# Kernel tuning notes

Hardware: AMD Instinct MI355X
Metric: run time of the kernel (lower is better)

The kernel has to match this reference:

```python
import jax, jax.numpy as jnp
import numpy as np

E = 2        # expan_att_chans
HEADS = 16   # num_chans * expan_att_chans


def _gconv1x1(x, w, b, groups):
    # Grouped 1x1 conv. x: [B, Cin, H, W]; w: [Cout, Cin//groups]; b: [Cout].
    # Output channel layout matches torch: group-major (c_group * gout + o).
    B, Cin, H, W = x.shape
    Cout = w.shape[0]
    gin, gout = Cin // groups, Cout // groups
    y = jnp.einsum('bgip,goi->bgop',
                   x.reshape(B, groups, gin, H * W),
                   w.reshape(groups, gout, gin))
    return y.reshape(B, Cout, H, W) + b[None, :, None, None]


def _l2norm(x, eps=1e-12):
    # F.normalize(dim=-1): x / max(||x||_2, eps)
    n = jnp.sqrt(jnp.sum(x * x, axis=-1, keepdims=True))
    return x / jnp.maximum(n, eps)


def setup_inputs() -> dict:
    key = jax.random.key(0)
    ks = jax.random.split(key, 12)
    B, C, H, W = 8, 128, 128, 128
    s = 0.05  # small init (module uses xavier gain=0.01)
    f32 = jnp.float32
    return {
        'x': jax.random.normal(ks[0], (B, C, H, W), f32),
        'to': jax.random.normal(ks[1], (B, C, H, W), f32),
        't': jnp.ones((1, HEADS, 1, 1), f32),
        # rgb qkv chain (fusion): C -> 2EC -> EC -> EC, all groups=C
        'w_r1': (jax.random.normal(ks[2], (C * E * 2, 1), f32) * s),
        'b_r1': jnp.zeros((C * E * 2,), f32),
        'w_r2': (jax.random.normal(ks[3], (C * E, 2 * E), f32) * s),
        'b_r2': jnp.zeros((C * E,), f32),
        'w_r3': (jax.random.normal(ks[4], (C * E, E), f32) * s),
        'b_r3': jnp.zeros((C * E,), f32),
        # text kv chain: C -> 2EC -> EC -> 2EC, all groups=C
        'w_t1': (jax.random.normal(ks[5], (C * E * 2, 1), f32) * s),
        'b_t1': jnp.zeros((C * E * 2,), f32),
        'w_t2': (jax.random.normal(ks[6], (C * E, 2 * E), f32) * s),
        'b_t2': jnp.zeros((C * E,), f32),
        'w_t3': (jax.random.normal(ks[7], (C * E * 2, E), f32) * s),
        'b_t3': jnp.zeros((C * E * 2,), f32),
        # fusion conv: Conv2d(E*C -> C, k=3, stride=1, pad=1) + LeakyReLU(0.2)
        'w_f': (jax.random.normal(ks[8], (C, C * E, 3, 3), f32) * 0.02),
        'b_f': jnp.zeros((C,), f32),
    }


def reference(x, to, t, w_r1, b_r1, w_r2, b_r2, w_r3, b_r3,
              w_t1, b_t1, w_t2, b_t2, w_t3, b_t3, w_f, b_f):
    B, C, H, W = x.shape
    Cexp = E * C
    d = Cexp // HEADS  # per-head channel dim
    HW = H * W

    # grouped 1x1 conv chains producing Q (from rgb) and K,V (from text)
    q = _gconv1x1(_gconv1x1(_gconv1x1(x, w_r1, b_r1, C), w_r2, b_r2, C), w_r3, b_r3, C)      # [B, EC, H, W]
    kv = _gconv1x1(_gconv1x1(_gconv1x1(to, w_t1, b_t1, C), w_t2, b_t2, C), w_t3, b_t3, C)    # [B, 2EC, H, W]

    # Rearrange 'B (C E) H W -> B E C H W' then view as [B, heads, d, HW]
    q = q.reshape(B, C, E, HW).transpose(0, 2, 1, 3).reshape(B, HEADS, d, HW)
    kv = kv.reshape(B, C, 2 * E, HW).transpose(0, 2, 1, 3)  # [B, 2E, C, HW]
    k = kv[:, :E].reshape(B, HEADS, d, HW)
    v = kv[:, E:].reshape(B, HEADS, d, HW)

    # channel (transposed) attention with L2-normalized Q,K and learned temperature
    qn, kn = _l2norm(q), _l2norm(k)
    attn = jax.nn.softmax(jnp.einsum('bhdp,bhep->bhde', qn, kn) * t, axis=-1)  # [B, H, d, d]
    xo = jnp.einsum('bhde,bhep->bhdp', attn, v)  # [B, heads, d, HW]

    # rearrange 'B C X (H W) -> B (X C) H W' with C=heads, X=d  (d-major, head-minor)
    xo = xo.transpose(0, 2, 1, 3).reshape(B, Cexp, H, W)

    # group_fus: 3x3 conv (stride 1, pad 1) + LeakyReLU(0.2), residual add
    y = jax.lax.conv_general_dilated(
        xo, w_f, window_strides=(1, 1), padding=((1, 1), (1, 1)),
        dimension_numbers=('NCHW', 'OIHW', 'NCHW'))
    y = jax.nn.leaky_relu(y + b_f[None, :, None, None], negative_slope=0.2)
    return x + y
```

## Files before the change

kernel.cpp:

```cpp
#include <hip/hip_runtime.h>
#include <math.h>

#define B_  8
#define C_  128
#define H_  128
#define W_  128
#define HW_ 16384

#define OFF_MPART 0
#define OFF_SPART 262144
#define OFF_M     327680
#define OFF_S     344064
#define OFF_WV    348160
#define OFF_CST   380928
#define OFF_T     382976
#define OFF_WEFF  392192
#define OFF_T2F   982016
#define T2_ROW    16640
#define T2_BATCH  2163200
#define WS_NEED   (982016ull * 4ull + 34611200ull)

typedef __attribute__((ext_vector_type(8))) short short8;
typedef __attribute__((ext_vector_type(4))) float f32x4;

__device__ __forceinline__ unsigned short f2bf(float f) {
  unsigned u = __float_as_uint(f);
  u += 0x7fffu + ((u >> 16) & 1u);
  return (unsigned short)(u >> 16);
}

__device__ __forceinline__ f32x4 mfma16(short8 a, short8 b, f32x4 c) {
  return __builtin_amdgcn_mfma_f32_16x16x32_bf16(a, b, c, 0, 0, 0);
}

__device__ __forceinline__ void gl16(const void* g, void* l) {
  const unsigned loff = (unsigned)(unsigned long long)l;
  __builtin_amdgcn_global_load_lds(
      (const __attribute__((address_space(1))) void*)g,
      (__attribute__((address_space(3))) void*)loff, 16, 0, 0);
}

__global__ __launch_bounds__(256) void k_gram(const float* __restrict__ x,
                                              const float* __restrict__ to,
                                              float* __restrict__ ws) {
  const int bid = blockIdx.x;
  const int ps  = bid & 15;
  const int blk = (bid >> 4) & 7;
  const int b   = bid >> 7;
  const int tid = threadIdx.x;
  const int w = tid >> 6, l = tid & 63;
  const int lm = l & 15, lh = l >> 4;
  const int c0 = blk * 16;

  const float* xc = x  + ((size_t)b * C_ + c0 + lm) * HW_;
  const float* tc = to + ((size_t)b * C_ + c0 + lm) * HW_;
  const int p0 = ps * 1024 + w * 256 + lh * 8;

  f32x4 acc = (f32x4)0.f;
  float sx = 0.f, sxx = 0.f, st = 0.f, stt = 0.f;
#pragma unroll
  for (int it = 0; it < 8; ++it) {
    const int p = p0 + it * 32;
    const f32x4 xa = *(const f32x4*)(xc + p);
    const f32x4 xb = *(const f32x4*)(xc + p + 4);
    const f32x4 ta = *(const f32x4*)(tc + p);
    const f32x4 tb = *(const f32x4*)(tc + p + 4);
    short8 xf, tf;
#pragma unroll
    for (int e = 0; e < 4; ++e) {
      xf[e]     = (short)f2bf(xa[e]);
      xf[4 + e] = (short)f2bf(xb[e]);
      tf[e]     = (short)f2bf(ta[e]);
      tf[4 + e] = (short)f2bf(tb[e]);
      sx += xa[e] + xb[e];
      sxx = fmaf(xa[e], xa[e], fmaf(xb[e], xb[e], sxx));
      st += ta[e] + tb[e];
      stt = fmaf(ta[e], ta[e], fmaf(tb[e], tb[e], stt));
    }
    acc = mfma16(xf, tf, acc);
  }

  sx  += __shfl_xor(sx, 16);  sx  += __shfl_xor(sx, 32);
  sxx += __shfl_xor(sxx, 16); sxx += __shfl_xor(sxx, 32);
  st  += __shfl_xor(st, 16);  st  += __shfl_xor(st, 32);
  stt += __shfl_xor(stt, 16); stt += __shfl_xor(stt, 32);

  __shared__ float smM[4][256];
  __shared__ float smS[4][4][16];
#pragma unroll
  for (int r = 0; r < 4; ++r)
    smM[w][(lh * 4 + r) * 16 + lm] = acc[r];
  if (l < 16) {
    smS[w][0][lm] = sx;  smS[w][1][lm] = sxx;
    smS[w][2][lm] = st;  smS[w][3][lm] = stt;
  }
  __syncthreads();

  {
    const float s = smM[0][tid & 255] + smM[1][tid & 255]
                  + smM[2][tid & 255] + smM[3][tid & 255];
    ws[OFF_MPART + (size_t)((b * 8 + blk) * 16 + ps) * 256 + tid] = s;
  }
  if (tid < 64) {
    const int kind = tid >> 4, ch = tid & 15;
    const float s = smS[0][kind][ch] + smS[1][kind][ch]
                  + smS[2][kind][ch] + smS[3][kind][ch];
    ws[OFF_SPART + (size_t)kind * 16384 + (size_t)(b * C_ + c0 + ch) * 16 + ps] = s;
  }
}

__global__ __launch_bounds__(256) void k_redB(float* __restrict__ ws) {
  const int gid = blockIdx.x * 256 + threadIdx.x;
  if (gid < 16384) {
    const float* mp = ws + OFF_MPART + (size_t)(gid >> 8) * 4096 + (gid & 255);
    float s = 0.f;
#pragma unroll
    for (int kc = 0; kc < 16; ++kc) s += mp[kc * 256];
    ws[OFF_M + gid] = s;
  } else {
    const int sidx = gid - 16384;
    const float* sp = ws + OFF_SPART + (size_t)sidx * 16;
    float s = 0.f;
#pragma unroll
    for (int kc = 0; kc < 16; ++kc) s += sp[kc];
    ws[OFF_S + sidx] = s;
  }
}

__global__ __launch_bounds__(256) void k_zero(unsigned short* __restrict__ t2) {
  const int b = blockIdx.x >> 1, r = blockIdx.x & 1;
  unsigned short* row = t2 + (size_t)b * T2_BATCH + (size_t)(r ? 129 : 0) * T2_ROW;
  const short8 z = {0,0,0,0,0,0,0,0};
  for (int idx = threadIdx.x; idx < 2080; idx += 256)
    *(short8*)(row + (size_t)idx * 8) = z;
}

__global__ __launch_bounds__(256) void k_tr(const float* __restrict__ to,
                                            unsigned short* __restrict__ t2) {
  const int d  = blockIdx.x;
  const int xh = d & 1;
  const int y  = (d >> 1) & 127;
  const int b  = d >> 8;
  const int tid = threadIdx.x;
  __shared__ char lds[64 * 256];

  const int x0 = xh * 64;
  const int xq = tid & 15;
  const int cg = tid >> 4;
  const float* srcb = to + ((size_t)b * C_ + cg * 8) * HW_ + (size_t)y * W_ + x0 + xq * 4;
#pragma unroll
  for (int k = 0; k < 8; ++k) {
    const f32x4 v = *(const f32x4*)(srcb + (size_t)k * HW_);
    const int c = cg * 8 + k;
#pragma unroll
    for (int e = 0; e < 4; ++e) {
      const int xl = xq * 4 + e;
      const int boff = xl * 256 + ((2 * c) ^ ((xl & 7) << 4));
      *(unsigned short*)(lds + boff) = f2bf(v[e]);
    }
  }
  __syncthreads();

  unsigned short* rowbase = t2 + (size_t)b * T2_BATCH + (size_t)(y + 1) * T2_ROW;
#pragma unroll
  for (int i = 0; i < 4; ++i) {
    const int xx = tid >> 2;
    const int cs = (tid & 3) + i * 4;
    short8 val = *(short8*)(lds + xx * 256 + ((cs * 16) ^ ((xx & 7) << 4)));
    *(short8*)(rowbase + (size_t)(x0 + xx + 1) * 128 + cs * 8) = val;
  }
  if (tid < 16) {
    short8 z = {0,0,0,0,0,0,0,0};
    if (xh == 0) *(short8*)(rowbase + tid * 8) = z;
    else         *(short8*)(rowbase + (size_t)129 * 128 + tid * 8) = z;
  }
}

__global__ __launch_bounds__(256) void k_attn(const float* __restrict__ t,
    const float* __restrict__ w_r1, const float* __restrict__ b_r1,
    const float* __restrict__ w_r2, const float* __restrict__ b_r2,
    const float* __restrict__ w_r3, const float* __restrict__ b_r3,
    const float* __restrict__ w_t1, const float* __restrict__ b_t1,
    const float* __restrict__ w_t2, const float* __restrict__ b_t2,
    const float* __restrict__ w_t3, const float* __restrict__ b_t3,
    float* __restrict__ ws) {
  const int b = blockIdx.x;
  const int tid = threadIdx.x;
  __shared__ float aQ[256], bQ[256], aK[256], bK[256], aV[256], bV[256];
  __shared__ float rks[256], kAs[256], kBs[256], stos[256];

  if (tid < 128) {
    const int g = tid;
    float A1[4], B1[4], A2[2], B2[2];
#pragma unroll
    for (int j = 0; j < 4; ++j) { A1[j] = w_r1[g * 4 + j]; B1[j] = b_r1[g * 4 + j]; }
#pragma unroll
    for (int i = 0; i < 2; ++i) {
      A2[i] = 0.f; B2[i] = b_r2[g * 2 + i];
#pragma unroll
      for (int j = 0; j < 4; ++j) {
        const float w = w_r2[(g * 2 + i) * 4 + j];
        A2[i] = fmaf(w, A1[j], A2[i]); B2[i] = fmaf(w, B1[j], B2[i]);
      }
    }
#pragma unroll
    for (int o = 0; o < 2; ++o) {
      float a = 0.f, bb = b_r3[g * 2 + o];
#pragma unroll
      for (int i = 0; i < 2; ++i) {
        const float w = w_r3[(g * 2 + o) * 2 + i];
        a = fmaf(w, A2[i], a); bb = fmaf(w, B2[i], bb);
      }
      aQ[g * 2 + o] = a; bQ[g * 2 + o] = bb;
    }
#pragma unroll
    for (int j = 0; j < 4; ++j) { A1[j] = w_t1[g * 4 + j]; B1[j] = b_t1[g * 4 + j]; }
#pragma unroll
    for (int i = 0; i < 2; ++i) {
      A2[i] = 0.f; B2[i] = b_t2[g * 2 + i];
#pragma unroll
      for (int j = 0; j < 4; ++j) {
        const float w = w_t2[(g * 2 + i) * 4 + j];
        A2[i] = fmaf(w, A1[j], A2[i]); B2[i] = fmaf(w, B1[j], B2[i]);
      }
    }
#pragma unroll
    for (int o = 0; o < 4; ++o) {
      float a = 0.f, bb = b_t3[g * 4 + o];
#pragma unroll
      for (int i = 0; i < 2; ++i) {
        const float w = w_t3[(g * 4 + o) * 2 + i];
        a = fmaf(w, A2[i], a); bb = fmaf(w, B2[i], bb);
      }
      if (o < 2) { aK[g * 2 + o] = a; bK[g * 2 + o] = bb; }
      else       { aV[g * 2 + (o - 2)] = a; bV[g * 2 + (o - 2)] = bb; }
    }
  }
  __syncthreads();

  const float* S   = ws + OFF_S;
  const float* Sx  = S;
  const float* Sxx = S + 1024;
  const float* Sto = S + 2048;
  const float* Stt = S + 3072;

  {
    const int h = tid >> 4, e = h >> 3, blk = h & 7, c0 = blk * 16;
    const int g = c0 + (tid & 15);
    const float a = aK[g * 2 + e], bb = bK[g * 2 + e];
    const float s2 = a * a * Stt[b * C_ + g] + 2.f * a * bb * Sto[b * C_ + g]
                   + bb * bb * 16384.f;
    rks[tid] = 1.f / fmaxf(sqrtf(fmaxf(s2, 0.f)), 1e-12f);
    kAs[tid] = a; kBs[tid] = bb;
    stos[tid] = Sto[b * C_ + g];
  }
  __syncthreads();

  {
    const int h = tid >> 4, i = tid & 15, e = h >> 3, blk = h & 7, c0 = blk * 16;
    const int gi = c0 + i;
    const float gA = aQ[gi * 2 + e], gB = bQ[gi * 2 + e];
    const float sxi = Sx[b * C_ + gi];
    const float q2 = gA * gA * Sxx[b * C_ + gi] + 2.f * gA * gB * sxi
                   + gB * gB * 16384.f;
    const float rnq = 1.f / fmaxf(sqrtf(fmaxf(q2, 0.f)), 1e-12f);
    const float tt = t[h];
    const float* Mrow = ws + OFF_M + (size_t)(b * 8 + blk) * 256 + i * 16;

    float lg[16];
    float mx = -1e30f;
#pragma unroll
    for (int j = 0; j < 16; ++j) {
      const float s = gA * kAs[h * 16 + j] * Mrow[j]
                    + gA * kBs[h * 16 + j] * sxi
                    + gB * kAs[h * 16 + j] * stos[h * 16 + j]
                    + gB * kBs[h * 16 + j] * 16384.f;
      const float l = tt * s * rnq * rks[h * 16 + j];
      lg[j] = l;
      mx = fmaxf(mx, l);
    }
    float den = 0.f;
#pragma unroll
    for (int j = 0; j < 16; ++j) { const float ev = expf(lg[j] - mx); lg[j] = ev; den += ev; }
    const float inv = 1.f / den;
    float cs = 0.f;
    float* WVp = ws + OFF_WV + (size_t)(b * 16 + h) * 256 + i * 16;
#pragma unroll
    for (int j = 0; j < 16; ++j) {
      const float aa = lg[j] * inv;
      const int gj = c0 + j;
      WVp[j] = aa * aV[gj * 2 + e];
      cs = fmaf(aa, bV[gj * 2 + e], cs);
    }
    ws[OFF_CST + b * 256 + i * 16 + h] = cs;
  }
}

__global__ __launch_bounds__(128) void k_weff(const float* __restrict__ w_f,
                                              float* __restrict__ ws) {
  const int b = blockIdx.x >> 7, oc = blockIdx.x & 127;
  const int c = threadIdx.x, blk = c >> 4, j = c & 15;
  const float* WVb = ws + OFF_WV;
  float acc[9];
#pragma unroll
  for (int k = 0; k < 9; ++k) acc[k] = 0.f;
#pragma unroll
  for (int e = 0; e < 2; ++e) {
    const int h = e * 8 + blk;
#pragma unroll
    for (int i = 0; i < 16; ++i) {
      const float coef = WVb[((size_t)(b * 16 + h) * 16 + i) * 16 + j];
      const float* wf = w_f + (size_t)(oc * 256 + i * 16 + h) * 9;
#pragma unroll
      for (int k = 0; k < 9; ++k) acc[k] = fmaf(wf[k], coef, acc[k]);
    }
  }
  unsigned short* wb16 = (unsigned short*)(ws + OFF_WEFF);
#pragma unroll
  for (int k = 0; k < 9; ++k)
    wb16[(((size_t)(b * 9 + k)) * 128 + oc) * 128 + c] = f2bf(acc[k]);

  __shared__ float tp[9][128];
  float tl[9];
#pragma unroll
  for (int k = 0; k < 9; ++k) tl[k] = 0.f;
  const float* cst = ws + OFF_CST + b * 256;
  for (int cc = c; cc < 256; cc += 128) {
    const float cv = cst[cc];
    const float* wf = w_f + (size_t)(oc * 256 + cc) * 9;
#pragma unroll
    for (int k = 0; k < 9; ++k) tl[k] = fmaf(wf[k], cv, tl[k]);
  }
#pragma unroll
  for (int k = 0; k < 9; ++k) tp[k][c] = tl[k];
  __syncthreads();
  for (int s = 64; s > 0; s >>= 1) {
    if (c < s) {
#pragma unroll
      for (int k = 0; k < 9; ++k) tp[k][c] += tp[k][c + s];
    }
    __syncthreads();
  }
  if (c < 9) ws[OFF_T + ((size_t)b * 128 + oc) * 9 + c] = tp[c][0];
}

__global__ __launch_bounds__(512, 2) void k_conv(const float* __restrict__ xin,
                                                 const float* __restrict__ b_f,
                                                 const float* __restrict__ ws,
                                                 const unsigned short* __restrict__ t2,
                                                 float* __restrict__ out) {
  const int d  = blockIdx.x;
  const int b  = d & 7;
  const int y2 = d >> 3;
  const int tid = threadIdx.x;

  __shared__ unsigned short B4s[33280];
  __shared__ unsigned short As[2][8192];

  const unsigned short* wb = (const unsigned short*)(ws + OFF_WEFF)
      + (size_t)b * 9 * 16384;
  const unsigned short* t2b4 = t2 + (size_t)b * T2_BATCH
      + (size_t)(y2 * 2) * T2_ROW;

  const int l = tid & 63;
  const int lm = l & 15, lh = l >> 4;
  const int wv = tid >> 6;
  const int oc0w = (wv & 1) * 64;
  const int px0w = ((wv >> 1) & 1) * 64;
  const int rw   = wv >> 2;

  const unsigned udstw = (unsigned)((tid & ~63) * 16);

#define STAGE_B4(KS)                                                           \
  {                                                                            \
    _Pragma("unroll")                                                          \
    for (int i_ = 0; i_ < 8; ++i_) {                                           \
      const int q_ = i_ * 512 + tid;                                           \
      const int rr_ = q_ / 1040;                                               \
      const int rem_ = q_ - rr_ * 1040;                                        \
      const int xi_ = rem_ >> 3, c8_ = rem_ & 7;                               \
      gl16(t2b4 + (size_t)rr_ * T2_ROW + xi_ * 128 + (KS) * 64                 \
               + ((c8_ ^ (xi_ & 7)) << 3),                                     \
           (char*)B4s + (unsigned)(i_ * 8192) + udstw);                        \
    }                                                                          \
    if (tid < 64) {                                                            \
      const int q_ = 4096 + tid;                                               \
      const int rr_ = q_ / 1040;                                               \
      const int rem_ = q_ - rr_ * 1040;                                        \
      const int xi_ = rem_ >> 3, c8_ = rem_ & 7;                               \
      gl16(t2b4 + (size_t)rr_ * T2_ROW + xi_ * 128 + (KS) * 64                 \
               + ((c8_ ^ (xi_ & 7)) << 3),                                     \
           (char*)B4s + 65536u);                                               \
    }                                                                          \
  }

#define STAGE_A(BUF, TAP, KS)                                                  \
  {                                                                            \
    const unsigned short* asrc = wb + (size_t)(TAP) * 16384 + (KS) * 64;       \
    _Pragma("unroll")                                                          \
    for (int k_ = 0; k_ < 2; ++k_) {                                           \
      const int task_ = k_ * 512 + tid;                                        \
      const int trow_ = task_ >> 3, c8_ = task_ & 7;                           \
      gl16(asrc + (size_t)trow_ * 128 + ((c8_ ^ (trow_ & 7)) << 3),            \
           (char*)&As[BUF][0] + (unsigned)(k_ * 8192) + udstw);                \
    }                                                                          \
  }

  f32x4 acc[4][4];
#pragma unroll
  for (int mt = 0; mt < 4; ++mt)
#pragma unroll
    for (int nt = 0; nt < 4; ++nt) acc[mt][nt] = (f32x4)0.f;

#pragma unroll 1
  for (int ks = 0; ks < 2; ++ks) {
    STAGE_B4(ks);
    STAGE_A(0, 0, ks);
    __syncthreads();

    int cur = 0;
#pragma unroll 1
    for (int tap = 0; tap < 9; ++tap) {
      if (tap + 1 < 9) STAGE_A(cur ^ 1, tap + 1, ks);

      const int dy = tap / 3, dx = tap - dy * 3;
      const int rdy = rw + dy;
      const char* Ab = (const char*)&As[cur][0];
      const char* Bb = (const char*)B4s;
#pragma unroll
      for (int ki = 0; ki < 2; ++ki) {
        short8 af[4], bfr[4];
#pragma unroll
        for (int mt = 0; mt < 4; ++mt) {
          const int oc = oc0w + mt * 16 + lm;
          af[mt] = *(const short8*)(Ab + oc * 128 + (((ki * 4 + lh) ^ (oc & 7)) << 4));
        }
#pragma unroll
        for (int nt = 0; nt < 4; ++nt) {
          const int xi = px0w + nt * 16 + lm + dx;
          bfr[nt] = *(const short8*)(Bb + (rdy * 130 + xi) * 128
                                        + (((ki * 4 + lh) ^ (xi & 7)) << 4));
        }
#pragma unroll
        for (int mt = 0; mt < 4; ++mt) {
          acc[mt][0] = mfma16(af[mt], bfr[0], acc[mt][0]);
          acc[mt][1] = mfma16(af[mt], bfr[1], acc[mt][1]);
          acc[mt][2] = mfma16(af[mt], bfr[2], acc[mt][2]);
          acc[mt][3] = mfma16(af[mt], bfr[3], acc[mt][3]);
        }
      }
      __syncthreads();
      cur ^= 1;
    }
  }
#undef STAGE_A
#undef STAGE_B4

  float* sm = (float*)B4s;
  if (tid < 256) {
    const int rr = tid >> 7, oc = tid & 127;
    const int y = y2 * 2 + rr;
    const float* Tk = ws + OFF_T + (size_t)(b * 128 + oc) * 9;
    float s = Tk[3] + Tk[4] + Tk[5], sl = Tk[3], sr = Tk[5];
    if (y >= 1)   { s += Tk[0] + Tk[1] + Tk[2]; sl += Tk[0]; sr += Tk[2]; }
    if (y <= 126) { s += Tk[6] + Tk[7] + Tk[8]; sl += Tk[6]; sr += Tk[8]; }
    sm[rr * 384 + oc] = s + b_f[oc];
    sm[rr * 384 + 128 + oc] = sl;
    sm[rr * 384 + 256 + oc] = sr;
  }
  __syncthreads();

  const int y = y2 * 2 + rw;
#pragma unroll
  for (int mt = 0; mt < 4; ++mt)
#pragma unroll
    for (int nt = 0; nt < 4; ++nt) {
      const int px = px0w + nt * 16 + lm;
#pragma unroll
      for (int r = 0; r < 4; ++r) {
        const int oc = oc0w + mt * 16 + lh * 4 + r;
        float add = sm[rw * 384 + oc];
        if (px == 0)   add -= sm[rw * 384 + 128 + oc];
        if (px == 127) add -= sm[rw * 384 + 256 + oc];
        const float z = acc[mt][nt][r] + add;
        const size_t base = ((size_t)(b * C_ + oc)) * HW_ + (size_t)y * W_ + px;
        const float rx = xin[base];
        out[base] = rx + (z >= 0.f ? z : 0.2f * z);
      }
    }
}

__global__ __launch_bounds__(512, 4) void k_conv_fb(const float* __restrict__ xin,
                                                    const float* __restrict__ to,
                                                    const float* __restrict__ b_f,
                                                    const float* __restrict__ ws,
                                                    float* __restrict__ out) {
  const int bid = blockIdx.x;
  const int nb  = (bid & 7) * 128 + (bid >> 3);
  const int b   = nb >> 7;
  const int y   = nb & 127;
  const int tid = threadIdx.x;

  __shared__ f32x4 ldsbuf[3120];
  char* lp = (char*)ldsbuf;

  f32x4 acc[4][2];
#pragma unroll
  for (int mt = 0; mt < 4; ++mt)
#pragma unroll
    for (int nt = 0; nt < 2; ++nt) acc[mt][nt] = (f32x4)0.f;

  const float* tob = to + (size_t)b * C_ * HW_;
  const unsigned short* wb16 =
      (const unsigned short*)(ws + OFF_WEFF) + (size_t)b * 9 * 128 * 128;

  const int l = tid & 63, wv = tid >> 6;
  const int ocb0 = (wv & 1) * 64, pxb0 = (wv >> 1) * 32;
  const int lm = l & 15, lh = l >> 4;

  for (int cb = 0; cb < 128; cb += 64) {
    __syncthreads();
    {
      const int xg = tid & 31, cq = (tid >> 5) & 15;
      const int cbase = cb + cq * 4;
#pragma unroll
      for (int row = 0; row < 3; ++row) {
        const int y_in = y + row - 1;
        const bool yok = ((unsigned)y_in < 128u);
        const float* src = tob + (size_t)cbase * HW_ + (size_t)y_in * W_;
#pragma unroll
        for (int xb = 0; xb < 5; ++xb) {
          const int xi = xb * 32 + xg;
          if (xi < 130) {
            const int x_in = xi - 1;
            const bool ok = yok && ((unsigned)x_in < 128u);
            float f0 = 0.f, f1 = 0.f, f2 = 0.f, f3 = 0.f;
            if (ok) {
              f0 = src[x_in];
              f1 = src[HW_ + x_in];
              f2 = src[2 * HW_ + x_in];
              f3 = src[3 * HW_ + x_in];
            }
            ushort4 pk;
            pk.x = f2bf(f0); pk.y = f2bf(f1); pk.z = f2bf(f2); pk.w = f2bf(f3);
            const int boff = (row * 130 + xi) * 128 + ((cq * 8) ^ ((xi & 7) << 4));
            *(ushort4*)(lp + boff) = pk;
          }
        }
      }
    }
    __syncthreads();

    for (int tap = 0; tap < 9; ++tap) {
      const int dy = tap / 3, dx = tap - dy * 3;
#pragma unroll
      for (int ks = 0; ks < 2; ++ks) {
        short8 bfr[2];
#pragma unroll
        for (int nt = 0; nt < 2; ++nt) {
          const int xi = pxb0 + nt * 16 + lm + dx;
          const int boff = (dy * 130 + xi) * 128 + ((ks * 64 + lh * 16) ^ ((xi & 7) << 4));
          bfr[nt] = *(const short8*)(lp + boff);
        }
        const int cin = cb + ks * 32 + lh * 8;
#pragma unroll
        for (int mt = 0; mt < 4; ++mt) {
          const int oc = ocb0 + mt * 16 + lm;
          const short8 af = *(const short8*)(wb16 + ((size_t)tap * 128 + oc) * 128 + cin);
          acc[mt][0] = mfma16(af, bfr[0], acc[mt][0]);
          acc[mt][1] = mfma16(af, bfr[1], acc[mt][1]);
        }
      }
    }
  }

  __syncthreads();
  float* sAdd = (float*)ldsbuf;
  float* sLft = sAdd + 128;
  float* sRgt = sAdd + 256;
  if (tid < 128) {
    const float* Tk = ws + OFF_T + (size_t)(b * 128 + tid) * 9;
    float s = Tk[3] + Tk[4] + Tk[5], sl = Tk[3], sr = Tk[5];
    if (y >= 1)   { s += Tk[0] + Tk[1] + Tk[2]; sl += Tk[0]; sr += Tk[2]; }
    if (y <= 126) { s += Tk[6] + Tk[7] + Tk[8]; sl += Tk[6]; sr += Tk[8]; }
    sAdd[tid] = s + b_f[tid]; sLft[tid] = sl; sRgt[tid] = sr;
  }
  __syncthreads();

#pragma unroll
  for (int mt = 0; mt < 4; ++mt)
#pragma unroll
    for (int nt = 0; nt < 2; ++nt) {
      const int px = pxb0 + nt * 16 + lm;
#pragma unroll
      for (int r = 0; r < 4; ++r) {
        const int oc = ocb0 + mt * 16 + lh * 4 + r;
        float add = sAdd[oc];
        if (px == 0)   add -= sLft[oc];
        if (px == 127) add -= sRgt[oc];
        const float z = acc[mt][nt][r] + add;
        const size_t base = ((size_t)(b * C_ + oc)) * HW_ + (size_t)y * W_ + px;
        const float rx = xin[base];
        out[base] = rx + (z >= 0.f ? z : 0.2f * z);
      }
    }
}

extern "C" void kernel_launch(void* const* d_in, const int* in_sizes, int n_in,
                              void* d_out, int out_size, void* d_ws, size_t ws_size,
                              hipStream_t stream) {
  (void)in_sizes; (void)n_in; (void)out_size;
  const float* x    = (const float*)d_in[0];
  const float* to   = (const float*)d_in[1];
  const float* t    = (const float*)d_in[2];
  const float* w_r1 = (const float*)d_in[3];
  const float* b_r1 = (const float*)d_in[4];
  const float* w_r2 = (const float*)d_in[5];
  const float* b_r2 = (const float*)d_in[6];
  const float* w_r3 = (const float*)d_in[7];
  const float* b_r3 = (const float*)d_in[8];
  const float* w_t1 = (const float*)d_in[9];
  const float* b_t1 = (const float*)d_in[10];
  const float* w_t2 = (const float*)d_in[11];
  const float* b_t2 = (const float*)d_in[12];
  const float* w_t3 = (const float*)d_in[13];
  const float* b_t3 = (const float*)d_in[14];
  const float* w_f  = (const float*)d_in[15];
  const float* b_f  = (const float*)d_in[16];
  float* ws  = (float*)d_ws;
  float* out = (float*)d_out;
  unsigned short* t2 = (unsigned short*)(ws + OFF_T2F);
  const bool fast = (ws_size >= WS_NEED);

  k_gram<<<1024, 256, 0, stream>>>(x, to, ws);
  k_redB<<<80, 256, 0, stream>>>(ws);
  if (fast) {
    k_zero<<<16, 256, 0, stream>>>(t2);
    k_tr<<<2048, 256, 0, stream>>>(to, t2);
  }
  k_attn<<<8, 256, 0, stream>>>(t, w_r1, b_r1, w_r2, b_r2, w_r3, b_r3,
                                w_t1, b_t1, w_t2, b_t2, w_t3, b_t3, ws);
  k_weff<<<1024, 128, 0, stream>>>(w_f, ws);
  if (fast) k_conv<<<512, 512, 0, stream>>>(x, b_f, ws, t2, out);
  else      k_conv_fb<<<1024, 512, 0, stream>>>(x, to, b_f, ws, out);
}
```

Measured before the change: 114.6 us.

## Fold partial-sum reduction into attention, merge zero/transpose kernels, split conv tiles by half-row

Removes the separate reduction kernel: the attention kernel now sums the Gram and statistic partials itself into shared memory. The zero-padding and transpose kernels become one launch, with the extra blocks doing the zeroing. The main conv kernel now splits each row pair into two 64-pixel halves, doubling the grid to 1024 blocks and halving the per-warp pixel tile and the B staging buffer. This cuts launch overhead and is meant to improve occupancy and load balance, at the cost of more redundant weight (A) staging per pixel and more halo reads.

New measurement: 111.3 us. -2.8%, faster.

```diff
diff --git a/kernel.cpp b/kernel.cpp
--- a/kernel.cpp
+++ b/kernel.cpp
@@ -9,8 +9,6 @@
 
 #define OFF_MPART 0
 #define OFF_SPART 262144
-#define OFF_M     327680
-#define OFF_S     344064
 #define OFF_WV    348160
 #define OFF_CST   380928
 #define OFF_T     382976
@@ -109,39 +107,22 @@
   }
 }
 
-__global__ __launch_bounds__(256) void k_redB(float* __restrict__ ws) {
-  const int gid = blockIdx.x * 256 + threadIdx.x;
-  if (gid < 16384) {
-    const float* mp = ws + OFF_MPART + (size_t)(gid >> 8) * 4096 + (gid & 255);
-    float s = 0.f;
-#pragma unroll
-    for (int kc = 0; kc < 16; ++kc) s += mp[kc * 256];
-    ws[OFF_M + gid] = s;
-  } else {
-    const int sidx = gid - 16384;
-    const float* sp = ws + OFF_SPART + (size_t)sidx * 16;
-    float s = 0.f;
-#pragma unroll
-    for (int kc = 0; kc < 16; ++kc) s += sp[kc];
-    ws[OFF_S + sidx] = s;
-  }
-}
-
-__global__ __launch_bounds__(256) void k_zero(unsigned short* __restrict__ t2) {
-  const int b = blockIdx.x >> 1, r = blockIdx.x & 1;
-  unsigned short* row = t2 + (size_t)b * T2_BATCH + (size_t)(r ? 129 : 0) * T2_ROW;
-  const short8 z = {0,0,0,0,0,0,0,0};
-  for (int idx = threadIdx.x; idx < 2080; idx += 256)
-    *(short8*)(row + (size_t)idx * 8) = z;
-}
-
-__global__ __launch_bounds__(256) void k_tr(const float* __restrict__ to,
-                                            unsigned short* __restrict__ t2) {
+__global__ __launch_bounds__(256) void k_trz(const float* __restrict__ to,
+                                             unsigned short* __restrict__ t2) {
   const int d  = blockIdx.x;
+  const int tid = threadIdx.x;
+  if (d >= 2048) {
+    const int e = d - 2048;
+    const int b = e >> 1, r = e & 1;
+    unsigned short* row = t2 + (size_t)b * T2_BATCH + (size_t)(r ? 129 : 0) * T2_ROW;
+    const short8 z = {0,0,0,0,0,0,0,0};
+    for (int idx = tid; idx < 2080; idx += 256)
+      *(short8*)(row + (size_t)idx * 8) = z;
+    return;
+  }
   const int xh = d & 1;
   const int y  = (d >> 1) & 127;
   const int b  = d >> 8;
-  const int tid = threadIdx.x;
   __shared__ char lds[64 * 256];
 
   const int x0 = xh * 64;
@@ -188,6 +169,28 @@
   const int tid = threadIdx.x;
   __shared__ float aQ[256], bQ[256], aK[256], bK[256], aV[256], bV[256];
   __shared__ float rks[256], kAs[256], kBs[256], stos[256];
+  __shared__ float Ms[2048];
+  __shared__ float Ss[512];
+
+#pragma unroll
+  for (int blk = 0; blk < 8; ++blk) {
+    const float* mp = ws + OFF_MPART + (size_t)((b * 8 + blk) * 16) * 256 + tid;
+    float s = 0.f;
+#pragma unroll
+    for (int ps = 0; ps < 16; ++ps) s += mp[ps * 256];
+    Ms[blk * 256 + tid] = s;
+  }
+#pragma unroll
+  for (int k2 = 0; k2 < 2; ++k2) {
+    const int idx = k2 * 256 + tid;
+    const int kind = idx >> 7, ch = idx & 127;
+    const float* sp = ws + OFF_SPART + (size_t)kind * 16384
+                    + (size_t)(b * C_ + ch) * 16;
+    float s = 0.f;
+#pragma unroll
+    for (int ps = 0; ps < 16; ++ps) s += sp[ps];
+    Ss[idx] = s;
+  }
 
   if (tid < 128) {
     const int g = tid;
@@ -238,21 +241,19 @@
   }
   __syncthreads();
 
-  const float* S   = ws + OFF_S;
-  const float* Sx  = S;
-  const float* Sxx = S + 1024;
-  const float* Sto = S + 2048;
-  const float* Stt = S + 3072;
+  const float* Sx  = Ss;
+  const float* Sxx = Ss + 128;
+  const float* Sto = Ss + 256;
+  const float* Stt = Ss + 384;
 
   {
     const int h = tid >> 4, e = h >> 3, blk = h & 7, c0 = blk * 16;
     const int g = c0 + (tid & 15);
     const float a = aK[g * 2 + e], bb = bK[g * 2 + e];
-    const float s2 = a * a * Stt[b * C_ + g] + 2.f * a * bb * Sto[b * C_ + g]
-                   + bb * bb * 16384.f;
+    const float s2 = a * a * Stt[g] + 2.f * a * bb * Sto[g] + bb * bb * 16384.f;
     rks[tid] = 1.f / fmaxf(sqrtf(fmaxf(s2, 0.f)), 1e-12f);
     kAs[tid] = a; kBs[tid] = bb;
-    stos[tid] = Sto[b * C_ + g];
+    stos[tid] = Sto[g];
   }
   __syncthreads();
 
@@ -260,12 +261,11 @@
     const int h = tid >> 4, i = tid & 15, e = h >> 3, blk = h & 7, c0 = blk * 16;
     const int gi = c0 + i;
     const float gA = aQ[gi * 2 + e], gB = bQ[gi * 2 + e];
-    const float sxi = Sx[b * C_ + gi];
-    const float q2 = gA * gA * Sxx[b * C_ + gi] + 2.f * gA * gB * sxi
-                   + gB * gB * 16384.f;
+    const float sxi = Sx[gi];
+    const float q2 = gA * gA * Sxx[gi] + 2.f * gA * gB * sxi + gB * gB * 16384.f;
     const float rnq = 1.f / fmaxf(sqrtf(fmaxf(q2, 0.f)), 1e-12f);
     const float tt = t[h];
-    const float* Mrow = ws + OFF_M + (size_t)(b * 8 + blk) * 256 + i * 16;
+    const float* Mrow = Ms + blk * 256 + i * 16;
 
     float lg[16];
     float mx = -1e30f;
@@ -351,46 +351,47 @@
                                                  float* __restrict__ out) {
   const int d  = blockIdx.x;
   const int b  = d & 7;
-  const int y2 = d >> 3;
+  const int xh = (d >> 3) & 1;
+  const int y2 = d >> 4;
   const int tid = threadIdx.x;
 
-  __shared__ unsigned short B4s[33280];
-  __shared__ unsigned short As[2][8192];
+  __shared__ unsigned short B4s[4 * 66 * 64];
+  __shared__ unsigned short As[2][128 * 64];
 
   const unsigned short* wb = (const unsigned short*)(ws + OFF_WEFF)
       + (size_t)b * 9 * 16384;
   const unsigned short* t2b4 = t2 + (size_t)b * T2_BATCH
-      + (size_t)(y2 * 2) * T2_ROW;
+      + (size_t)(y2 * 2) * T2_ROW + (size_t)(xh * 64) * 128;
 
   const int l = tid & 63;
   const int lm = l & 15, lh = l >> 4;
   const int wv = tid >> 6;
-  const int oc0w = (wv & 1) * 64;
-  const int px0w = ((wv >> 1) & 1) * 64;
   const int rw   = wv >> 2;
+  const int oc0w = ((wv >> 1) & 1) * 64;
+  const int px0  = (wv & 1) * 32;
 
   const unsigned udstw = (unsigned)((tid & ~63) * 16);
 
 #define STAGE_B4(KS)                                                           \
   {                                                                            \
     _Pragma("unroll")                                                          \
-    for (int i_ = 0; i_ < 8; ++i_) {                                           \
+    for (int i_ = 0; i_ < 4; ++i_) {                                           \
       const int q_ = i_ * 512 + tid;                                           \
-      const int rr_ = q_ / 1040;                                               \
-      const int rem_ = q_ - rr_ * 1040;                                        \
+      const int rr_ = q_ / 528;                                                \
+      const int rem_ = q_ - rr_ * 528;                                         \
       const int xi_ = rem_ >> 3, c8_ = rem_ & 7;                               \
       gl16(t2b4 + (size_t)rr_ * T2_ROW + xi_ * 128 + (KS) * 64                 \
                + ((c8_ ^ (xi_ & 7)) << 3),                                     \
            (char*)B4s + (unsigned)(i_ * 8192) + udstw);                        \
     }                                                                          \
     if (tid < 64) {                                                            \
-      const int q_ = 4096 + tid;                                               \
-      const int rr_ = q_ / 1040;                                               \
-      const int rem_ = q_ - rr_ * 1040;                                        \
+      const int q_ = 2048 + tid;                                               \
+      const int rr_ = q_ / 528;                                                \
+      const int rem_ = q_ - rr_ * 528;                                         \
       const int xi_ = rem_ >> 3, c8_ = rem_ & 7;                               \
       gl16(t2b4 + (size_t)rr_ * T2_ROW + xi_ * 128 + (KS) * 64                 \
                + ((c8_ ^ (xi_ & 7)) << 3),                                     \
-           (char*)B4s + 65536u);                                               \
+           (char*)B4s + 32768u);                                               \
     }                                                                          \
   }
 
@@ -406,11 +407,9 @@
     }                                                                          \
   }
 
-  f32x4 acc[4][4];
-#pragma unroll
-  for (int mt = 0; mt < 4; ++mt)
-#pragma unroll
-    for (int nt = 0; nt < 4; ++nt) acc[mt][nt] = (f32x4)0.f;
+  f32x4 acc[4][2];
+#pragma unroll
+  for (int mt = 0; mt < 4; ++mt) { acc[mt][0] = (f32x4)0.f; acc[mt][1] = (f32x4)0.f; }
 
 #pragma unroll 1
   for (int ks = 0; ks < 2; ++ks) {
@@ -429,24 +428,22 @@
       const char* Bb = (const char*)B4s;
 #pragma unroll
       for (int ki = 0; ki < 2; ++ki) {
-        short8 af[4], bfr[4];
+        short8 af[4], bfr[2];
 #pragma unroll
         for (int mt = 0; mt < 4; ++mt) {
           const int oc = oc0w + mt * 16 + lm;
           af[mt] = *(const short8*)(Ab + oc * 128 + (((ki * 4 + lh) ^ (oc & 7)) << 4));
         }
 #pragma unroll
-        for (int nt = 0; nt < 4; ++nt) {
-          const int xi = px0w + nt * 16 + lm + dx;
-          bfr[nt] = *(const short8*)(Bb + (rdy * 130 + xi) * 128
+        for (int nt = 0; nt < 2; ++nt) {
+          const int xi = px0 + nt * 16 + lm + dx;
+          bfr[nt] = *(const short8*)(Bb + (rdy * 66 + xi) * 128
                                         + (((ki * 4 + lh) ^ (xi & 7)) << 4));
         }
 #pragma unroll
         for (int mt = 0; mt < 4; ++mt) {
           acc[mt][0] = mfma16(af[mt], bfr[0], acc[mt][0]);
           acc[mt][1] = mfma16(af[mt], bfr[1], acc[mt][1]);
-          acc[mt][2] = mfma16(af[mt], bfr[2], acc[mt][2]);
-          acc[mt][3] = mfma16(af[mt], bfr[3], acc[mt][3]);
         }
       }
       __syncthreads();
@@ -474,8 +471,8 @@
 #pragma unroll
   for (int mt = 0; mt < 4; ++mt)
 #pragma unroll
-    for (int nt = 0; nt < 4; ++nt) {
-      const int px = px0w + nt * 16 + lm;
+    for (int nt = 0; nt < 2; ++nt) {
+      const int px = xh * 64 + px0 + nt * 16 + lm;
 #pragma unroll
       for (int r = 0; r < 4; ++r) {
         const int oc = oc0w + mt * 16 + lh * 4 + r;
@@ -633,14 +630,10 @@
   const bool fast = (ws_size >= WS_NEED);
 
   k_gram<<<1024, 256, 0, stream>>>(x, to, ws);
-  k_redB<<<80, 256, 0, stream>>>(ws);
-  if (fast) {
-    k_zero<<<16, 256, 0, stream>>>(t2);
-    k_tr<<<2048, 256, 0, stream>>>(to, t2);
-  }
+  if (fast) k_trz<<<2064, 256, 0, stream>>>(to, t2);
   k_attn<<<8, 256, 0, stream>>>(t, w_r1, b_r1, w_r2, b_r2, w_r3, b_r3,
                                 w_t1, b_t1, w_t2, b_t2, w_t3, b_t3, ws);
   k_weff<<<1024, 128, 0, stream>>>(w_f, ws);
-  if (fast) k_conv<<<512, 512, 0, stream>>>(x, b_f, ws, t2, out);
+  if (fast) k_conv<<<1024, 512, 0, stream>>>(x, b_f, ws, t2, out);
   else      k_conv_fb<<<1024, 512, 0, stream>>>(x, to, b_f, ws, out);
 }
```
